# Kernel optimization log

Measured on AMD Instinct MI355X. Metric: run time of the kernel, lower is better.

## Reference

```python
import jax, jax.numpy as jnp
import numpy as np

B, C, H, W = 512, 2048, 8, 8   # batch, backbone channels, feature-map HxW (cfg.output_hm_shape)
J = 30                          # smpl.pos_joint_num
CF = 512                        # conv output channels
EPS = 1e-5                      # BatchNorm eps


def setup_inputs() -> dict:
    key = jax.random.key(0)
    ks = jax.random.split(key, 10)
    D = J * (CF + 3)  # 15450
    return {
        "img_feat": jax.random.normal(ks[0], (B, C, H, W), jnp.float32),
        # joint coords in heatmap pixel space [0, W-1] (x, y, z)
        "joint_coord_img": jax.random.uniform(ks[1], (B, J, 3), jnp.float32) * (W - 1),
        "conv_w": jax.random.normal(ks[2], (CF, C), jnp.float32) * 0.02,
        "conv_b": jnp.zeros((CF,), jnp.float32),
        "bn_gamma": jnp.ones((CF,), jnp.float32),
        "bn_beta": jnp.zeros((CF,), jnp.float32),
        "bn_mean": jnp.zeros((CF,), jnp.float32),
        "bn_var": jnp.ones((CF,), jnp.float32),
        "root_w": jax.random.normal(ks[3], (6, D), jnp.float32) * 0.01,
        "root_b": jnp.zeros((6,), jnp.float32),
        "pose_w": jax.random.normal(ks[4], (126, D), jnp.float32) * 0.01,
        "pose_b": jnp.zeros((126,), jnp.float32),
        "shape_w": jax.random.normal(ks[5], (10, C), jnp.float32) * 0.01,
        "shape_b": jnp.zeros((10,), jnp.float32),
        "cam_w": jax.random.normal(ks[6], (3, C), jnp.float32) * 0.01,
        "cam_b": jnp.zeros((3,), jnp.float32),
    }


def _bilinear_sample(feat, xy):
    """Batched bilinear sample == F.grid_sample(align_corners=True, padding='zeros')
    with grid built directly from pixel coords in [0, W-1].
    feat: (B, Cf, H, W), xy: (B, J, 2) pixel coords -> (B, J, Cf)."""
    x, y = xy[..., 0], xy[..., 1]
    x0f, y0f = jnp.floor(x), jnp.floor(y)
    wx1, wy1 = x - x0f, y - y0f
    wx0, wy0 = 1.0 - wx1, 1.0 - wy1
    x0, y0 = x0f.astype(jnp.int32), y0f.astype(jnp.int32)
    x1, y1 = x0 + 1, y0 + 1

    def corner(yi, xi, wt):
        valid = (xi >= 0) & (xi < feat.shape[3]) & (yi >= 0) & (yi < feat.shape[2])
        yc = jnp.clip(yi, 0, feat.shape[2] - 1)
        xc = jnp.clip(xi, 0, feat.shape[3] - 1)
        # gather (B, Cf, J) via vmap over batch
        g = jax.vmap(lambda f, yy, xx: f[:, yy, xx])(feat, yc, xc)
        return g * (wt * valid.astype(feat.dtype))[:, None, :]

    out = (corner(y0, x0, wy0 * wx0) + corner(y0, x1, wy0 * wx1)
           + corner(y1, x0, wy1 * wx0) + corner(y1, x1, wy1 * wx1))
    return jnp.transpose(out, (0, 2, 1))  # (B, J, Cf)


def reference(img_feat, joint_coord_img, conv_w, conv_b, bn_gamma, bn_beta,
              bn_mean, bn_var, root_w, root_b, pose_w, pose_b,
              shape_w, shape_b, cam_w, cam_b):
    bsz = img_feat.shape[0]
    pooled = img_feat.mean(axis=(2, 3))                       # (B, 2048)
    shape_param = pooled @ shape_w.T + shape_b                # (B, 10)
    cam_param = pooled @ cam_w.T + cam_b                      # (B, 3)

    # 1x1 conv + BatchNorm (eval) + ReLU
    f = jnp.einsum('bchw,oc->bohw', img_feat, conv_w) + conv_b[None, :, None, None]
    f = (f - bn_mean[None, :, None, None]) * jax.lax.rsqrt(bn_var + EPS)[None, :, None, None]
    f = jax.nn.relu(f * bn_gamma[None, :, None, None] + bn_beta[None, :, None, None])

    # fused per-joint bilinear gather (replaces the per-joint python loop)
    img_feat_joints = _bilinear_sample(f, joint_coord_img[..., :2])  # (B, J, 512)
    feat = jnp.concatenate([img_feat_joints, joint_coord_img], axis=2)  # (B, J, 515)
    feat = feat.reshape(bsz, -1)                              # (B, 15450)

    root_pose = feat @ root_w.T + root_b                      # (B, 6)
    pose_param = feat @ pose_w.T + pose_b                     # (B, 126)
    return (root_pose, pose_param, shape_param, cam_param)
```

## Files before the change

### kernel.cpp

```cpp
#include <hip/hip_runtime.h>
#include <stdint.h>

typedef __attribute__((ext_vector_type(8))) short bf16x8;
typedef __attribute__((ext_vector_type(4))) float f32x4;

__device__ __forceinline__ unsigned short f2bf(float f) {
    union { float f; uint32_t u; } v; v.f = f;
    uint32_t r = (v.u + 0x7FFFu + ((v.u >> 16) & 1u)) >> 16;
    return (unsigned short)r;
}
__device__ __forceinline__ float bf2f(unsigned short u) {
    union { uint32_t u; float f; } v; v.u = ((uint32_t)u) << 16; return v.f;
}

__device__ __forceinline__ void gload16(const void* g, void* l) {
    __builtin_amdgcn_global_load_lds(
        (const __attribute__((address_space(1))) unsigned int*)g,
        (__attribute__((address_space(3))) unsigned int*)l, 16, 0, 0);
}

#define WP_ELEMS  1081344
#define K2        15456
#define W2P_ELEMS (144 * K2)

#define ABUF0  0
#define ABUF1  33792
#define BBUF0  67584
#define BBUF1  71680
#define REDOFF 75776
#define SMEM_SZ 76032

__global__ void pack_convw_kernel(const float* __restrict__ cw,
                                  const float* __restrict__ sw,
                                  const float* __restrict__ camw,
                                  unsigned short* __restrict__ Wp) {
    int gid = blockIdx.x * 256 + threadIdx.x;
    if (gid >= WP_ELEMS) return;
    int kt  = gid / 16896;
    int rem = gid - kt * 16896;
    int g   = rem >> 9;
    int r2  = rem & 511;
    int q   = r2 >> 7;
    int rr  = (r2 >> 3) & 15;
    int e   = r2 & 7;
    int row = g * 16 + rr;
    int k   = kt * 32 + q * 8 + e;
    float v = 0.f;
    if (row < 512)      v = cw[row * 2048 + k];
    else if (row < 522) v = sw[(row - 512) * 2048 + k];
    else if (row < 525) v = camw[(row - 522) * 2048 + k];
    Wp[gid] = f2bf(v);
}

__global__ void pack_w2_kernel(const float* __restrict__ root_w,
                               const float* __restrict__ pose_w,
                               unsigned short* __restrict__ W2p) {
    int gid = blockIdx.x * 256 + threadIdx.x;
    if (gid >= W2P_ELEMS) return;
    int o2 = gid / K2;
    int kk = gid - o2 * K2;
    float v = 0.f;
    if (o2 < 132) {
        const float* wr = (o2 < 6) ? (root_w + o2 * 15450) : (pose_w + (o2 - 6) * 15450);
        if (kk < 15360) {
            int j = kk >> 9;
            int o = kk & 511;
            v = wr[j * 515 + o];
        } else {
            int c = kk - 15360;
            if (c < 90) {
                int j = c / 3, d = c - 3 * j;
                v = wr[j * 515 + 512 + d];
            }
        }
    }
    W2p[gid] = f2bf(v);
}

__global__ void bn_prep_kernel(const float* cb, const float* g, const float* be,
                               const float* m, const float* v, float* sbws) {
    int o = blockIdx.x * 256 + threadIdx.x;
    if (o >= 512) return;
    float s = g[o] * rsqrtf(v[o] + 1e-5f);
    sbws[2 * o]     = s;
    sbws[2 * o + 1] = be[o] + s * (cb[o] - m[o]);
}

__global__ __launch_bounds__(256, 2)
void conv_main_kernel(const float* __restrict__ img,
                      const float* __restrict__ jc,
                      const unsigned short* __restrict__ Wp,
                      const float* __restrict__ sbws,
                      const float* __restrict__ shape_b,
                      const float* __restrict__ cam_b,
                      unsigned short* __restrict__ sampled,
                      float* __restrict__ out) {
    __shared__ __align__(16) char smem[SMEM_SZ];
    const int t    = threadIdx.x;
    const int lane = t & 63;
    const int w    = t >> 6;
    const int l15  = lane & 15;
    const int quad = lane >> 4;
    const int b    = blockIdx.x;

    f32x4 acc[8][4];
    f32x4 accX;
    #pragma unroll
    for (int mi = 0; mi < 8; ++mi)
        #pragma unroll
        for (int nt = 0; nt < 4; ++nt)
            acc[mi][nt] = (f32x4){0.f, 0.f, 0.f, 0.f};
    accX = (f32x4){0.f, 0.f, 0.f, 0.f};

    const float* gBbase = img + (size_t)b * 131072 + (size_t)(w * 8) * 64 + lane;
    float fb[8];

    auto loadB = [&](int kt) {
        const float* gB = gBbase + (size_t)(kt * 32) * 64;
        #pragma unroll
        for (int j = 0; j < 8; ++j) fb[j] = gB[j * 64];
    };
    auto writeB = [&](char* bbuf) {
        int4 bv;
        bv.x = (int)((uint32_t)f2bf(fb[0]) | ((uint32_t)f2bf(fb[1]) << 16));
        bv.y = (int)((uint32_t)f2bf(fb[2]) | ((uint32_t)f2bf(fb[3]) << 16));
        bv.z = (int)((uint32_t)f2bf(fb[4]) | ((uint32_t)f2bf(fb[5]) << 16));
        bv.w = (int)((uint32_t)f2bf(fb[6]) | ((uint32_t)f2bf(fb[7]) << 16));
        *(int4*)(bbuf + (lane >> 4) * 1024 + w * 256 + l15 * 16) = bv;
    };
    auto stageA = [&](int kt, char* abuf) {
        const unsigned short* src = Wp + (size_t)kt * 16896 + (size_t)(w * 8) * 512 + lane * 8;
        char* dst = abuf + w * 8192;
        #pragma unroll
        for (int i = 0; i < 8; ++i)
            gload16(src + i * 512, dst + i * 1024);
        if (w == 0)
            gload16(Wp + (size_t)kt * 16896 + 32 * 512 + lane * 8, abuf + 32768);
    };
    auto compute = [&](const char* abuf, const char* bbuf) {
        bf16x8 bfr0 = *(const bf16x8*)(bbuf + 0 * 1024 + quad * 256 + l15 * 16);
        bf16x8 bfr1 = *(const bf16x8*)(bbuf + 1 * 1024 + quad * 256 + l15 * 16);
        bf16x8 bfr2 = *(const bf16x8*)(bbuf + 2 * 1024 + quad * 256 + l15 * 16);
        bf16x8 bfr3 = *(const bf16x8*)(bbuf + 3 * 1024 + quad * 256 + l15 * 16);
        #pragma unroll
        for (int mi = 0; mi < 8; ++mi) {
            bf16x8 afr = *(const bf16x8*)(abuf + (w * 8 + mi) * 1024 + quad * 256 + l15 * 16);
            acc[mi][0] = __builtin_amdgcn_mfma_f32_16x16x32_bf16(afr, bfr0, acc[mi][0], 0, 0, 0);
            acc[mi][1] = __builtin_amdgcn_mfma_f32_16x16x32_bf16(afr, bfr1, acc[mi][1], 0, 0, 0);
            acc[mi][2] = __builtin_amdgcn_mfma_f32_16x16x32_bf16(afr, bfr2, acc[mi][2], 0, 0, 0);
            acc[mi][3] = __builtin_amdgcn_mfma_f32_16x16x32_bf16(afr, bfr3, acc[mi][3], 0, 0, 0);
        }
        {
            bf16x8 afrX = *(const bf16x8*)(abuf + 32768 + quad * 256 + l15 * 16);
            bf16x8 bfrW = *(const bf16x8*)(bbuf + w * 1024 + quad * 256 + l15 * 16);
            accX = __builtin_amdgcn_mfma_f32_16x16x32_bf16(afrX, bfrW, accX, 0, 0, 0);
        }
    };

    loadB(0);
    stageA(0, smem + ABUF0);
    writeB(smem + BBUF0);
    __syncthreads();

    #pragma unroll 2
    for (int kt = 0; kt < 64; ++kt) {
        char* acur = smem + ((kt & 1) ? ABUF1 : ABUF0);
        char* bcur = smem + ((kt & 1) ? BBUF1 : BBUF0);
        char* anxt = smem + ((kt & 1) ? ABUF0 : ABUF1);
        char* bnxt = smem + ((kt & 1) ? BBUF0 : BBUF1);
        if (kt < 63) {
            loadB(kt + 1);
            stageA(kt + 1, anxt);
        }
        compute(acur, bcur);
        if (kt < 63) writeB(bnxt);
        __syncthreads();
    }

    const float2* sb2 = (const float2*)sbws;
    #pragma unroll
    for (int mi = 0; mi < 8; ++mi) {
        #pragma unroll
        for (int r = 0; r < 4; ++r) {
            int row = w * 128 + mi * 16 + quad * 4 + r;
            float2 sb = sb2[row];
            #pragma unroll
            for (int nt = 0; nt < 4; ++nt) {
                int col = nt * 16 + l15;
                float v = fmaxf(acc[mi][nt][r] * sb.x + sb.y, 0.f);
                *(unsigned short*)(smem + row * 128 + (((col + row) & 63) << 1)) = f2bf(v);
            }
        }
    }
    float* red = (float*)(smem + REDOFF);
    #pragma unroll
    for (int r = 0; r < 4; ++r) {
        float v = accX[r];
        v += __shfl_xor(v, 1);
        v += __shfl_xor(v, 2);
        v += __shfl_xor(v, 4);
        v += __shfl_xor(v, 8);
        if (l15 == 0) red[w * 16 + quad * 4 + r] = v;
    }
    __syncthreads();

    if (t < 16) {
        float v = (red[t] + red[16 + t] + red[32 + t] + red[48 + t]) * 0.015625f;
        if (t < 10)      out[67584 + b * 10 + t] = v + shape_b[t];
        else if (t < 13) out[72704 + b * 3 + (t - 10)] = v + cam_b[t - 10];
    }
    const float* jcb = jc + b * 90;
    if (t < 96) {
        float v = (t < 90) ? jcb[t] : 0.f;
        sampled[(size_t)b * K2 + 15360 + t] = f2bf(v);
    }

    unsigned int* outsamp = (unsigned int*)(sampled + (size_t)b * K2);
    const int o = 2 * t;
    for (int s = 0; s < 30; ++s) {
        float x = jcb[s * 3 + 0];
        float y = jcb[s * 3 + 1];
        float x0f = floorf(x), y0f = floorf(y);
        int x0 = (int)x0f, y0 = (int)y0f;
        int x1 = x0 + 1, y1 = y0 + 1;
        float wx1 = x - x0f, wy1 = y - y0f;
        float wx0 = 1.f - wx1, wy0 = 1.f - wy1;
        float vx0 = (x0 >= 0 && x0 < 8) ? 1.f : 0.f;
        float vx1 = (x1 >= 0 && x1 < 8) ? 1.f : 0.f;
        float vy0 = (y0 >= 0 && y0 < 8) ? 1.f : 0.f;
        float vy1 = (y1 >= 0 && y1 < 8) ? 1.f : 0.f;
        int cx0 = min(max(x0, 0), 7), cx1 = min(max(x1, 0), 7);
        int cy0 = min(max(y0, 0), 7), cy1 = min(max(y1, 0), 7);
        int p00 = cy0 * 8 + cx0, p01 = cy0 * 8 + cx1;
        int p10 = cy1 * 8 + cx0, p11 = cy1 * 8 + cx1;
        float w00 = wy0 * wx0 * vy0 * vx0, w01 = wy0 * wx1 * vy0 * vx1;
        float w10 = wy1 * wx0 * vy1 * vx0, w11 = wy1 * wx1 * vy1 * vx1;
        float vA = w00 * bf2f(*(unsigned short*)(smem + o * 128 + (((p00 + o) & 63) << 1)))
                 + w01 * bf2f(*(unsigned short*)(smem + o * 128 + (((p01 + o) & 63) << 1)))
                 + w10 * bf2f(*(unsigned short*)(smem + o * 128 + (((p10 + o) & 63) << 1)))
                 + w11 * bf2f(*(unsigned short*)(smem + o * 128 + (((p11 + o) & 63) << 1)));
        int o1 = o + 1;
        float vB = w00 * bf2f(*(unsigned short*)(smem + o1 * 128 + (((p00 + o1) & 63) << 1)))
                 + w01 * bf2f(*(unsigned short*)(smem + o1 * 128 + (((p01 + o1) & 63) << 1)))
                 + w10 * bf2f(*(unsigned short*)(smem + o1 * 128 + (((p10 + o1) & 63) << 1)))
                 + w11 * bf2f(*(unsigned short*)(smem + o1 * 128 + (((p11 + o1) & 63) << 1)));
        outsamp[s * 256 + t] = (uint32_t)f2bf(vA) | ((uint32_t)f2bf(vB) << 16);
    }
}

__global__ __launch_bounds__(256, 4)
void gemm2_kernel(const unsigned short* __restrict__ sampled,
                  const unsigned short* __restrict__ W2p,
                  float* __restrict__ part) {
    __shared__ __align__(16) char smem[16640];
    const int t    = threadIdx.x;
    const int lane = t & 63;
    const int w    = t >> 6;
    const int l15  = lane & 15;
    const int quad = lane >> 4;
    const int m0   = blockIdx.x * 64;
    const int j    = blockIdx.y;
    const int k0   = j * 512;
    const int ktn  = (j == 30) ? 3 : 16;

    f32x4 acc[9];
    #pragma unroll
    for (int nt = 0; nt < 9; ++nt) acc[nt] = (f32x4){0.f, 0.f, 0.f, 0.f};

    for (int kt = 0; kt < ktn; ++kt) {
        __syncthreads();
        {
            int r = t >> 2, ci = t & 3;
            int4 d = *(const int4*)(sampled + (size_t)(m0 + r) * K2 + k0 + kt * 32 + ci * 8);
            *(int4*)(smem + r * 80 + ci * 16) = d;
        }
        #pragma unroll
        for (int i = 0; i < 3; ++i) {
            int c2 = t + 256 * i;
            if (c2 < 576) {
                int r = c2 >> 2, ci = c2 & 3;
                int4 d = *(const int4*)(W2p + (size_t)r * K2 + k0 + kt * 32 + ci * 8);
                *(int4*)(smem + 5120 + r * 80 + ci * 16) = d;
            }
        }
        __syncthreads();
        bf16x8 a = *(const bf16x8*)(smem + (w * 16 + l15) * 80 + quad * 16);
        #pragma unroll
        for (int nt = 0; nt < 9; ++nt) {
            bf16x8 bfv = *(const bf16x8*)(smem + 5120 + (nt * 16 + l15) * 80 + quad * 16);
            acc[nt] = __builtin_amdgcn_mfma_f32_16x16x32_bf16(a, bfv, acc[nt], 0, 0, 0);
        }
    }
    float* pout = part + (size_t)(j * 8 + blockIdx.x) * 9216;
    #pragma unroll
    for (int nt = 0; nt < 9; ++nt) {
        #pragma unroll
        for (int r = 0; r < 4; ++r) {
            pout[(w * 16 + quad * 4 + r) * 144 + nt * 16 + l15] = acc[nt][r];
        }
    }
}

__global__ void reduce_out_kernel(const float* __restrict__ part,
                                  const float* __restrict__ root_b,
                                  const float* __restrict__ pose_b,
                                  float* __restrict__ out) {
    int gid = blockIdx.x * 256 + threadIdx.x;
    int m  = gid / 132;
    int o2 = gid - m * 132;
    float s = (o2 < 6) ? root_b[o2] : pose_b[o2 - 6];
    const float* p = part + (size_t)(m >> 6) * 9216 + (m & 63) * 144 + o2;
    #pragma unroll
    for (int j = 0; j < 31; ++j) s += p[(size_t)j * 8 * 9216];
    if (o2 < 6) out[m * 6 + o2] = s;
    else        out[3072 + m * 126 + (o2 - 6)] = s;
}

extern "C" void kernel_launch(void* const* d_in, const int* in_sizes, int n_in,
                              void* d_out, int out_size, void* d_ws, size_t ws_size,
                              hipStream_t stream) {
    const float* img     = (const float*)d_in[0];
    const float* jc      = (const float*)d_in[1];
    const float* conv_w  = (const float*)d_in[2];
    const float* conv_b  = (const float*)d_in[3];
    const float* bn_g    = (const float*)d_in[4];
    const float* bn_be   = (const float*)d_in[5];
    const float* bn_m    = (const float*)d_in[6];
    const float* bn_v    = (const float*)d_in[7];
    const float* root_w  = (const float*)d_in[8];
    const float* root_b  = (const float*)d_in[9];
    const float* pose_w  = (const float*)d_in[10];
    const float* pose_b  = (const float*)d_in[11];
    const float* shape_w = (const float*)d_in[12];
    const float* shape_b = (const float*)d_in[13];
    const float* cam_w   = (const float*)d_in[14];
    const float* cam_b   = (const float*)d_in[15];
    float* out = (float*)d_out;
    char* ws = (char*)d_ws;

    unsigned short* Wp   = (unsigned short*)(ws);
    unsigned short* W2p  = (unsigned short*)(ws + 2162688);
    unsigned short* samp = (unsigned short*)(ws + 6614016);
    float* part          = (float*)(ws + 22440960);
    float* sbws          = (float*)(ws + 31583232);

    pack_convw_kernel<<<4224, 256, 0, stream>>>(conv_w, shape_w, cam_w, Wp);
    pack_w2_kernel<<<8694, 256, 0, stream>>>(root_w, pose_w, W2p);
    bn_prep_kernel<<<2, 256, 0, stream>>>(conv_b, bn_g, bn_be, bn_m, bn_v, sbws);
    conv_main_kernel<<<512, 256, 0, stream>>>(img, jc, Wp, sbws, shape_b, cam_b,
                                              samp, out);
    gemm2_kernel<<<dim3(8, 31), 256, 0, stream>>>(samp, W2p, part);
    reduce_out_kernel<<<264, 256, 0, stream>>>(part, root_b, pose_b, out);
}
```

Before: 471.2 us.

## Deepen conv GEMM prefetch with double register buffers and merge prep kernels

The main conv kernel now holds two register buffers for the image tile, so global loads run two k-steps ahead. It uses explicit vmcnt waits and raw barriers instead of __syncthreads, which lets outstanding loads stay in flight across the barrier. The loop is manually unrolled by two with fixed LDS buffers, and every wave now issues the extra A-row load, not just wave 0. The three weight and BN prep kernels are merged into one launch to cut launch overhead. The risks are higher register pressure at two blocks per CU and hand-counted waitcnt values that must match the number of loads issued.

Result: no change. 464.2 us (-1.5%).

```diff
diff --git a/kernel.cpp b/kernel.cpp
--- a/kernel.cpp
+++ b/kernel.cpp
@@ -30,60 +30,67 @@
 #define REDOFF 75776
 #define SMEM_SZ 76032
 
-__global__ void pack_convw_kernel(const float* __restrict__ cw,
-                                  const float* __restrict__ sw,
-                                  const float* __restrict__ camw,
-                                  unsigned short* __restrict__ Wp) {
+#define WAIT_VM8 asm volatile("s_waitcnt vmcnt(8) lgkmcnt(0)" ::: "memory")
+#define WAIT_VM0 asm volatile("s_waitcnt vmcnt(0) lgkmcnt(0)" ::: "memory")
+#define BAR do { __builtin_amdgcn_s_barrier(); __builtin_amdgcn_sched_barrier(0); } while (0)
+
+__global__ void prep_kernel(const float* __restrict__ cw,
+                            const float* __restrict__ sw,
+                            const float* __restrict__ camw,
+                            const float* __restrict__ root_w,
+                            const float* __restrict__ pose_w,
+                            const float* __restrict__ cb, const float* __restrict__ g,
+                            const float* __restrict__ be, const float* __restrict__ m,
+                            const float* __restrict__ vv,
+                            unsigned short* __restrict__ Wp,
+                            unsigned short* __restrict__ W2p,
+                            float* __restrict__ sbws) {
     int gid = blockIdx.x * 256 + threadIdx.x;
-    if (gid >= WP_ELEMS) return;
-    int kt  = gid / 16896;
-    int rem = gid - kt * 16896;
-    int g   = rem >> 9;
-    int r2  = rem & 511;
-    int q   = r2 >> 7;
-    int rr  = (r2 >> 3) & 15;
-    int e   = r2 & 7;
-    int row = g * 16 + rr;
-    int k   = kt * 32 + q * 8 + e;
-    float v = 0.f;
-    if (row < 512)      v = cw[row * 2048 + k];
-    else if (row < 522) v = sw[(row - 512) * 2048 + k];
-    else if (row < 525) v = camw[(row - 522) * 2048 + k];
-    Wp[gid] = f2bf(v);
-}
-
-__global__ void pack_w2_kernel(const float* __restrict__ root_w,
-                               const float* __restrict__ pose_w,
-                               unsigned short* __restrict__ W2p) {
-    int gid = blockIdx.x * 256 + threadIdx.x;
-    if (gid >= W2P_ELEMS) return;
-    int o2 = gid / K2;
-    int kk = gid - o2 * K2;
-    float v = 0.f;
-    if (o2 < 132) {
-        const float* wr = (o2 < 6) ? (root_w + o2 * 15450) : (pose_w + (o2 - 6) * 15450);
-        if (kk < 15360) {
-            int j = kk >> 9;
-            int o = kk & 511;
-            v = wr[j * 515 + o];
-        } else {
-            int c = kk - 15360;
-            if (c < 90) {
-                int j = c / 3, d = c - 3 * j;
-                v = wr[j * 515 + 512 + d];
+    if (gid < WP_ELEMS) {
+        int kt  = gid / 16896;
+        int rem = gid - kt * 16896;
+        int gg  = rem >> 9;
+        int r2  = rem & 511;
+        int q   = r2 >> 7;
+        int rr  = (r2 >> 3) & 15;
+        int e   = r2 & 7;
+        int row = gg * 16 + rr;
+        int k   = kt * 32 + q * 8 + e;
+        float v = 0.f;
+        if (row < 512)      v = cw[row * 2048 + k];
+        else if (row < 522) v = sw[(row - 512) * 2048 + k];
+        else if (row < 525) v = camw[(row - 522) * 2048 + k];
+        Wp[gid] = f2bf(v);
+        return;
+    }
+    gid -= WP_ELEMS;
+    if (gid < W2P_ELEMS) {
+        int o2 = gid / K2;
+        int kk = gid - o2 * K2;
+        float v = 0.f;
+        if (o2 < 132) {
+            const float* wr = (o2 < 6) ? (root_w + o2 * 15450) : (pose_w + (o2 - 6) * 15450);
+            if (kk < 15360) {
+                int j = kk >> 9;
+                int o = kk & 511;
+                v = wr[j * 515 + o];
+            } else {
+                int c = kk - 15360;
+                if (c < 90) {
+                    int j = c / 3, d = c - 3 * j;
+                    v = wr[j * 515 + 512 + d];
+                }
             }
         }
-    }
-    W2p[gid] = f2bf(v);
-}
-
-__global__ void bn_prep_kernel(const float* cb, const float* g, const float* be,
-                               const float* m, const float* v, float* sbws) {
-    int o = blockIdx.x * 256 + threadIdx.x;
-    if (o >= 512) return;
-    float s = g[o] * rsqrtf(v[o] + 1e-5f);
-    sbws[2 * o]     = s;
-    sbws[2 * o + 1] = be[o] + s * (cb[o] - m[o]);
+        W2p[gid] = f2bf(v);
+        return;
+    }
+    gid -= W2P_ELEMS;
+    if (gid < 512) {
+        float s = g[gid] * rsqrtf(vv[gid] + 1e-5f);
+        sbws[2 * gid]     = s;
+        sbws[2 * gid + 1] = be[gid] + s * (cb[gid] - m[gid]);
+    }
 }
 
 __global__ __launch_bounds__(256, 2)
@@ -113,14 +120,14 @@
     accX = (f32x4){0.f, 0.f, 0.f, 0.f};
 
     const float* gBbase = img + (size_t)b * 131072 + (size_t)(w * 8) * 64 + lane;
-    float fb[8];
-
-    auto loadB = [&](int kt) {
+    float fbA[8], fbB[8];
+
+    auto loadB = [&](int kt, float* fb) {
         const float* gB = gBbase + (size_t)(kt * 32) * 64;
         #pragma unroll
         for (int j = 0; j < 8; ++j) fb[j] = gB[j * 64];
     };
-    auto writeB = [&](char* bbuf) {
+    auto writeB = [&](const float* fb, char* bbuf) {
         int4 bv;
         bv.x = (int)((uint32_t)f2bf(fb[0]) | ((uint32_t)f2bf(fb[1]) << 16));
         bv.y = (int)((uint32_t)f2bf(fb[2]) | ((uint32_t)f2bf(fb[3]) << 16));
@@ -129,13 +136,13 @@
         *(int4*)(bbuf + (lane >> 4) * 1024 + w * 256 + l15 * 16) = bv;
     };
     auto stageA = [&](int kt, char* abuf) {
-        const unsigned short* src = Wp + (size_t)kt * 16896 + (size_t)(w * 8) * 512 + lane * 8;
+        const unsigned short* base = Wp + (size_t)kt * 16896;
+        const unsigned short* src  = base + (size_t)(w * 8) * 512 + lane * 8;
         char* dst = abuf + w * 8192;
         #pragma unroll
         for (int i = 0; i < 8; ++i)
             gload16(src + i * 512, dst + i * 1024);
-        if (w == 0)
-            gload16(Wp + (size_t)kt * 16896 + 32 * 512 + lane * 8, abuf + 32768);
+        gload16(base + 32 * 512 + lane * 8, abuf + 32768);
     };
     auto compute = [&](const char* abuf, const char* bbuf) {
         bf16x8 bfr0 = *(const bf16x8*)(bbuf + 0 * 1024 + quad * 256 + l15 * 16);
@@ -157,26 +164,35 @@
         }
     };
 
-    loadB(0);
+    loadB(0, fbA);
     stageA(0, smem + ABUF0);
-    writeB(smem + BBUF0);
+    loadB(1, fbB);
+    writeB(fbA, smem + BBUF0);
+    WAIT_VM8;
+    BAR;
+
+    #pragma unroll 1
+    for (int kt = 0; kt < 64; kt += 2) {
+        {
+            if (kt < 63) stageA(kt + 1, smem + ABUF1);
+            if (kt < 62) loadB(kt + 2, fbA);
+            compute(smem + ABUF0, smem + BBUF0);
+            if (kt < 63) writeB(fbB, smem + BBUF1);
+            if (kt < 62) { WAIT_VM8; } else { WAIT_VM0; }
+            BAR;
+        }
+        {
+            int k1 = kt + 1;
+            if (k1 < 63) stageA(k1 + 1, smem + ABUF0);
+            if (k1 < 62) loadB(k1 + 2, fbB);
+            compute(smem + ABUF1, smem + BBUF1);
+            if (k1 < 63) writeB(fbA, smem + BBUF0);
+            if (k1 < 62) { WAIT_VM8; } else { WAIT_VM0; }
+            BAR;
+        }
+    }
+
     __syncthreads();
-
-    #pragma unroll 2
-    for (int kt = 0; kt < 64; ++kt) {
-        char* acur = smem + ((kt & 1) ? ABUF1 : ABUF0);
-        char* bcur = smem + ((kt & 1) ? BBUF1 : BBUF0);
-        char* anxt = smem + ((kt & 1) ? ABUF0 : ABUF1);
-        char* bnxt = smem + ((kt & 1) ? BBUF0 : BBUF1);
-        if (kt < 63) {
-            loadB(kt + 1);
-            stageA(kt + 1, anxt);
-        }
-        compute(acur, bcur);
-        if (kt < 63) writeB(bnxt);
-        __syncthreads();
-    }
-
     const float2* sb2 = (const float2*)sbws;
     #pragma unroll
     for (int mi = 0; mi < 8; ++mi) {
@@ -344,9 +360,9 @@
     float* part          = (float*)(ws + 22440960);
     float* sbws          = (float*)(ws + 31583232);
 
-    pack_convw_kernel<<<4224, 256, 0, stream>>>(conv_w, shape_w, cam_w, Wp);
-    pack_w2_kernel<<<8694, 256, 0, stream>>>(root_w, pose_w, W2p);
-    bn_prep_kernel<<<2, 256, 0, stream>>>(conv_b, bn_g, bn_be, bn_m, bn_v, sbws);
+    prep_kernel<<<12920, 256, 0, stream>>>(conv_w, shape_w, cam_w, root_w, pose_w,
+                                           conv_b, bn_g, bn_be, bn_m, bn_v,
+                                           Wp, W2p, sbws);
     conv_main_kernel<<<512, 256, 0, stream>>>(img, jc, Wp, sbws, shape_b, cam_b,
                                               samp, out);
     gemm2_kernel<<<dim3(8, 31), 256, 0, stream>>>(samp, W2p, part);
```
